# Performance work log

Hardware: AMD Instinct MI355X
Metric: run time of the kernel (lower is better)

Reference implementation:

```python
import jax, jax.numpy as jnp
import numpy as np


def setup_inputs() -> dict:
    key = jax.random.key(0)
    B, L, H, D = 4, 4096, 8, 64
    sample_k = int(np.ceil(np.log(L)))  # factor=1 -> U_part = ceil(ln L_K) = 9
    k1, k2, k3, k4 = jax.random.split(key, 4)
    return {
        "queries": jax.random.normal(k1, (B, L, H, D), jnp.float32),
        "keys": jax.random.normal(k2, (B, L, H, D), jnp.float32),
        "values": jax.random.normal(k3, (B, L, H, D), jnp.float32),
        "index_sample": jax.random.randint(k4, (L, sample_k), 0, L),
    }


def _prob_attention(Q, K, V, index_sample):
    # Q, K, V: [B, H, L, D]
    B, H, L_K, D = K.shape
    L_Q = Q.shape[2]
    u = min(int(np.ceil(np.log(L_Q))), L_Q)  # n_top (static)

    # --- _prob_QK: sampled scores, sparsity measure M, top-u queries ---
    # gather sampled keys per query position: [B, H, L_Q, sample_k, D]
    K_sample = K[:, :, index_sample, :]
    QK_sample = jnp.einsum('bhld,bhlsd->bhls', Q, K_sample)  # [B,H,L_Q,S]
    M = QK_sample.max(axis=-1) - QK_sample.sum(axis=-1) / L_K  # [B,H,L_Q]
    _, M_top = jax.lax.top_k(M, u)  # [B,H,u] indices of top queries

    Q_reduce = jnp.take_along_axis(Q, M_top[..., None], axis=2)  # [B,H,u,D]
    scale = 1.0 / jnp.sqrt(jnp.asarray(D, Q.dtype))
    scores = jnp.einsum('bhud,bhkd->bhuk', Q_reduce, K) * scale  # [B,H,u,L_K]

    # --- initial context (mask_flag=False): mean of V over keys ---
    context = jnp.broadcast_to(V.mean(axis=2, keepdims=True), (B, H, L_Q, D))

    # --- update context at the top-u query positions ---
    attn = jax.nn.softmax(scores, axis=-1)  # [B,H,u,L_K]
    ctx_top = jnp.einsum('bhuk,bhkd->bhud', attn, V)  # [B,H,u,D]
    b_idx = jnp.arange(B)[:, None, None]
    h_idx = jnp.arange(H)[None, :, None]
    context = context.at[b_idx, h_idx, M_top].set(ctx_top)
    return context, attn


def reference(queries, keys, values, index_sample):
    # inputs: [B, L, H, D] -> internal [B, H, L, D]
    Q = queries.transpose(0, 2, 1, 3)
    K = keys.transpose(0, 2, 1, 3)
    V = values.transpose(0, 2, 1, 3)
    context, attn = _prob_attention(Q, K, V, index_sample)
    return context.transpose(0, 2, 1, 3), attn
```

## Files before the change

kernel.cpp:

```cpp
#include <hip/hip_runtime.h>
#include <math.h>

#define B_ 4
#define L_ 4096
#define H_ 8
#define D_ 64
#define S_ 9
#define U_ 9
#define VC_ 64
#define NC_ 32
#define CC_ 16
#define TKC_ 8

#define MB2_ 8192
#define FILLBLK_ 8192

__device__ __forceinline__ float dot4(const float4& a, const float4& b) {
    return a.x * b.x + a.y * b.y + a.z * b.z + a.w * b.w;
}

__global__ void kernel_Mv(const float* __restrict__ Q, const float* __restrict__ K,
                          const int* __restrict__ idx, float* __restrict__ M,
                          const float* __restrict__ V, float* __restrict__ vpart) {
    __shared__ __align__(16) char smem[8192];
    int t = threadIdx.x;

    if (blockIdx.x >= MB2_) {
        int blk = blockIdx.x - MB2_;
        int c = blk & (VC_ - 1), b = blk >> 6;
        float4* red = (float4*)smem;
        float4 acc = make_float4(0.f, 0.f, 0.f, 0.f);
        int col = t & 127, lp = t >> 7;
        if (t < 512) {
            const float4* base = (const float4*)(V + (size_t)b * L_ * H_ * D_);
            for (int l = c * 64 + lp; l < (c + 1) * 64; l += 4) {
                float4 v = base[(size_t)l * 128 + col];
                acc.x += v.x; acc.y += v.y; acc.z += v.z; acc.w += v.w;
            }
            red[t] = acc;
        }
        __syncthreads();
        if (t < 128) {
            float4 r0 = red[t], r1 = red[t + 128], r2 = red[t + 256], r3 = red[t + 384];
            float4 o = make_float4(r0.x + r1.x + r2.x + r3.x, r0.y + r1.y + r2.y + r3.y,
                                   r0.z + r1.z + r2.z + r3.z, r0.w + r1.w + r2.w + r3.w);
            ((float4*)vpart)[(size_t)blk * 128 + t] = o;
        }
        return;
    }
    int n = blockIdx.x;
    int x = n & 7, m = n >> 3;
    int chunk = m & 255;
    int bh = (m >> 8) * 8 + x;
    int h = bh & (H_ - 1), b = bh >> 3;
    int l0 = chunk * 16;

    int j  = t & 3;
    int g  = t >> 2;
    int s  = g >> 4;
    int ll = g & 15;
    int l  = l0 + ll;

    int ki = idx[l * S_ + s];
    const float4* qb = (const float4*)(Q + (size_t)((b * L_ + l) * H_ + h) * D_);
    const float4* kb = (const float4*)(K + (size_t)((b * L_ + ki) * H_ + h) * D_);

    float acc = 0.0f;
#pragma unroll
    for (int c = 0; c < 4; ++c) acc += dot4(qb[j + 4 * c], kb[j + 4 * c]);
    acc += __shfl_xor(acc, 1);
    acc += __shfl_xor(acc, 2);

    float (*sdot)[S_] = (float (*)[S_])smem;
    if (j == 0) sdot[ll][s] = acc;
    __syncthreads();

    if (t < 16) {
        float mx = -INFINITY, sm = 0.0f;
#pragma unroll
        for (int ss = 0; ss < S_; ++ss) {
            float v = sdot[t][ss];
            mx = fmaxf(mx, v);
            sm += v;
        }
        M[((size_t)bh << 12) + l0 + t] = mx - sm * (1.0f / (float)L_);
    }
}

#define CSWAP(a, b)                                                          \
    if (v[b] > v[a] || (v[b] == v[a] && id[b] < id[a])) {                    \
        float tv = v[a]; v[a] = v[b]; v[b] = tv;                             \
        int ti = id[a]; id[a] = id[b]; id[b] = ti;                           \
    }

__global__ void kernel_topk(const float* __restrict__ M, int* __restrict__ Mtop,
                            const float* __restrict__ vpart, float* __restrict__ vmean) {
    int t = threadIdx.x;
    if (blockIdx.x >= 32) {
        int bh = blockIdx.x - 32;
        if (t < 64) {
            int h = bh & (H_ - 1), b = bh >> 3;
            float s = 0.0f;
            for (int c = 0; c < VC_; ++c)
                s += vpart[(size_t)(b * VC_ + c) * (H_ * D_) + h * D_ + t];
            vmean[bh * D_ + t] = s * (1.0f / (float)L_);
        }
        return;
    }
    int bh = blockIdx.x;
    int w = t >> 6, lane = t & 63;
    __shared__ float cvs[TKC_ * U_];
    __shared__ int   cis[TKC_ * U_];
    const float* Ms = M + ((size_t)bh << 12);

    {
        float v[8]; int id[8];
#pragma unroll
        for (int c = 0; c < 8; ++c) {
            int gi = w * 512 + lane + 64 * c;
            v[c] = Ms[gi]; id[c] = gi;
        }
        CSWAP(0,1) CSWAP(2,3) CSWAP(4,5) CSWAP(6,7)
        CSWAP(0,2) CSWAP(1,3) CSWAP(4,6) CSWAP(5,7)
        CSWAP(1,2) CSWAP(5,6)
        CSWAP(0,4) CSWAP(1,5) CSWAP(2,6) CSWAP(3,7)
        CSWAP(2,4) CSWAP(3,5)
        CSWAP(1,2) CSWAP(3,4) CSWAP(5,6)
#pragma unroll
        for (int r = 0; r < U_; ++r) {
            float bv = v[0]; int bi = id[0];
#pragma unroll
            for (int off = 1; off < 64; off <<= 1) {
                float ov = __shfl_xor(bv, off);
                int   oi = __shfl_xor(bi, off);
                if (ov > bv || (ov == bv && oi < bi)) { bv = ov; bi = oi; }
            }
            if (lane == 0) { cvs[w * U_ + r] = bv; cis[w * U_ + r] = bi; }
            if (id[0] == bi) {
#pragma unroll
                for (int c = 0; c < 7; ++c) { v[c] = v[c+1]; id[c] = id[c+1]; }
                v[7] = -INFINITY; id[7] = 0x7fffffff;
            }
        }
    }
    __syncthreads();
    if (w == 0) {
        float v[2]; int id[2];
        v[0] = cvs[lane]; id[0] = cis[lane];
        if (lane < TKC_ * U_ - 64) { v[1] = cvs[64 + lane]; id[1] = cis[64 + lane]; }
        else { v[1] = -INFINITY; id[1] = 0x7fffffff; }
        CSWAP(0,1)
#pragma unroll
        for (int r = 0; r < U_; ++r) {
            float bv = v[0]; int bi = id[0];
#pragma unroll
            for (int off = 1; off < 64; off <<= 1) {
                float ov = __shfl_xor(bv, off);
                int   oi = __shfl_xor(bi, off);
                if (ov > bv || (ov == bv && oi < bi)) { bv = ov; bi = oi; }
            }
            if (lane == 0) Mtop[bh * U_ + r] = bi;
            if (id[0] == bi) { v[0] = v[1]; id[0] = id[1]; v[1] = -INFINITY; id[1] = 0x7fffffff; }
        }
    }
}

__global__ void kernel_fill_scores(float* __restrict__ out, const float* __restrict__ vmean,
                                   const float* __restrict__ Q, const float* __restrict__ K,
                                   const int* __restrict__ Mtop, float* __restrict__ raw,
                                   float* __restrict__ spart) {
    int t = threadIdx.x;
    if (blockIdx.x < FILLBLK_) {
        int i = blockIdx.x * 256 + t;
        int d4 = i & 15;
        int h  = (i >> 4) & (H_ - 1);
        int l  = (i >> 7) & (L_ - 1);
        int b  = i >> 19;
        int bh = b * H_ + h;
        bool top = false;
#pragma unroll
        for (int u = 0; u < U_; ++u) top |= (Mtop[bh * U_ + u] == l);
        float4 w = top ? make_float4(0.f, 0.f, 0.f, 0.f)
                       : ((const float4*)vmean)[bh * 16 + d4];
        ((float4*)out)[i] = w;
        return;
    }
    int n = blockIdx.x - FILLBLK_;
    int x = n & 7, m = n >> 3;
    int chunk = m & (NC_ - 1);
    int bh = (m >> 5) * 8 + x;
    int h = bh & (H_ - 1), b = bh >> 3;
    int k0 = chunk * (L_ / NC_);

    __shared__ float qs[U_][D_];
    __shared__ float wsum[4][U_];
    if (t < 144) {
        int u = t / 16, c = t & 15;
        int l = Mtop[bh * U_ + u];
        ((float4*)qs[u])[c] =
            ((const float4*)(Q + (size_t)((b * L_ + l) * H_ + h) * D_))[c];
    }
    __syncthreads();

    int j = t & 3, g = t >> 2;
    float el[U_];
#pragma unroll
    for (int u = 0; u < U_; ++u) el[u] = 0.0f;

#pragma unroll
    for (int kk = 0; kk < 2; ++kk) {
        int k = k0 + g + 64 * kk;
        const float4* kb = (const float4*)(K + (size_t)((b * L_ + k) * H_ + h) * D_);
        float4 kv[4];
#pragma unroll
        for (int c = 0; c < 4; ++c) kv[c] = kb[j + 4 * c];
#pragma unroll
        for (int u = 0; u < U_; ++u) {
            float acc = 0.0f;
#pragma unroll
            for (int c = 0; c < 4; ++c)
                acc += dot4(((const float4*)qs[u])[j + 4 * c], kv[c]);
            acc += __shfl_xor(acc, 1);
            acc += __shfl_xor(acc, 2);
            float e = expf(acc * 0.125f);
            el[u] += e;
            if (j == 0) raw[((size_t)bh * U_ + u) * L_ + k] = e;
        }
    }
    int wv = t >> 6, lane = t & 63;
#pragma unroll
    for (int u = 0; u < U_; ++u) {
        float e = el[u];
#pragma unroll
        for (int off = 1; off < 64; off <<= 1)
            e += __shfl_xor(e, off);
        if (lane == 0) wsum[wv][u] = e * 0.25f;
    }
    __syncthreads();
    if (t < U_) {
        float s = wsum[0][t] + wsum[1][t] + wsum[2][t] + wsum[3][t];
        spart[(size_t)(bh * U_ + t) * NC_ + chunk] = s;
    }
}

__global__ void kernel_ctxf(float* __restrict__ attn, const float* __restrict__ V,
                            const int* __restrict__ Mtop, const float* __restrict__ spart,
                            float* __restrict__ out) {
    int n = blockIdx.x;
    int x = n & 7, m = n >> 3;
    int chunk = m & (CC_ - 1);
    int bh = (m >> 4) * 8 + x;
    int h = bh & (H_ - 1), b = bh >> 3;
    int k0 = chunk * (L_ / CC_);
    int t = threadIdx.x;

    __shared__ float sA[U_][256];
    __shared__ float4 red4[U_][4][16];
    __shared__ float sinvL[U_];

    if (t < U_) {
        const float* sp = spart + (size_t)(bh * U_ + t) * NC_;
        float s = 0.0f;
#pragma unroll
        for (int c = 0; c < NC_; ++c) s += sp[c];
        sinvL[t] = 1.0f / s;
    }
    __syncthreads();

    float* abase = attn + (size_t)bh * U_ * L_;
#pragma unroll
    for (int u = 0; u < U_; ++u) {
        float e = abase[(size_t)u * L_ + k0 + t] * sinvL[u];
        abase[(size_t)u * L_ + k0 + t] = e;
        sA[u][t] = e;
    }
    __syncthreads();

    int g = t >> 6, lane = t & 63;
    int kl = lane >> 4, d4 = lane & 15;

    float4 acc[U_];
#pragma unroll
    for (int u = 0; u < U_; ++u) acc[u] = make_float4(0.f, 0.f, 0.f, 0.f);

    for (int i = 0; i < 16; ++i) {
        int kloc = (g * 4 + kl) + 16 * i;
        float4 vv = *(const float4*)(V + (size_t)((b * L_ + k0 + kloc) * H_ + h) * D_ + 4 * d4);
#pragma unroll
        for (int u = 0; u < U_; ++u) {
            float av = sA[u][kloc];
            acc[u].x += av * vv.x; acc[u].y += av * vv.y;
            acc[u].z += av * vv.z; acc[u].w += av * vv.w;
        }
    }
#pragma unroll
    for (int u = 0; u < U_; ++u) {
        acc[u].x += __shfl_xor(acc[u].x, 16); acc[u].y += __shfl_xor(acc[u].y, 16);
        acc[u].z += __shfl_xor(acc[u].z, 16); acc[u].w += __shfl_xor(acc[u].w, 16);
        acc[u].x += __shfl_xor(acc[u].x, 32); acc[u].y += __shfl_xor(acc[u].y, 32);
        acc[u].z += __shfl_xor(acc[u].z, 32); acc[u].w += __shfl_xor(acc[u].w, 32);
    }
    if (kl == 0) {
#pragma unroll
        for (int u = 0; u < U_; ++u) red4[u][g][d4] = acc[u];
    }
    __syncthreads();
    if (t < U_ * 16) {
        int u = t >> 4, dd = t & 15;
        float4 s0 = red4[u][0][dd], s1 = red4[u][1][dd];
        float4 s2 = red4[u][2][dd], s3 = red4[u][3][dd];
        int lq = Mtop[bh * U_ + u];
        float* o = out + (size_t)((b * L_ + lq) * H_ + h) * D_ + 4 * dd;
        atomicAdd(o + 0, s0.x + s1.x + s2.x + s3.x);
        atomicAdd(o + 1, s0.y + s1.y + s2.y + s3.y);
        atomicAdd(o + 2, s0.z + s1.z + s2.z + s3.z);
        atomicAdd(o + 3, s0.w + s1.w + s2.w + s3.w);
    }
}

extern "C" void kernel_launch(void* const* d_in, const int* in_sizes, int n_in,
                              void* d_out, int out_size, void* d_ws, size_t ws_size,
                              hipStream_t stream) {
    const float* Q   = (const float*)d_in[0];
    const float* K   = (const float*)d_in[1];
    const float* V   = (const float*)d_in[2];
    const int*   idx = (const int*)d_in[3];

    float* ctx_out  = (float*)d_out;
    float* attn_out = (float*)d_out + (size_t)B_ * L_ * H_ * D_;

    float* M      = (float*)d_ws;
    float* vpart  = M + (size_t)B_ * H_ * L_;
    float* vmean  = vpart + (size_t)B_ * VC_ * H_ * D_;
    int*   Mtop   = (int*)(vmean + B_ * H_ * D_);
    float* spart  = (float*)(Mtop + 32 * U_);

    kernel_Mv<<<MB2_ + B_ * VC_, 576, 0, stream>>>(Q, K, idx, M, V, vpart);
    kernel_topk<<<64, 512, 0, stream>>>(M, Mtop, vpart, vmean);
    kernel_fill_scores<<<FILLBLK_ + 32 * NC_, 256, 0, stream>>>(
        ctx_out, vmean, Q, K, Mtop, attn_out, spart);
    kernel_ctxf<<<32 * CC_, 256, 0, stream>>>(attn_out, V, Mtop, spart, ctx_out);
}
```

Baseline: 233.9 us.

## Fuse score and context kernels using last-block-done normalization

Merges the score/exp kernel with the attention-times-V context kernel. Each score block now computes the unnormalized exp weights times V for its key chunk and atomically accumulates the result into a workspace buffer. An atomic counter lets the last block per (b,h) normalize the attention rows and write the final context rows. This removes one kernel launch and the separate re-read of attention scores, but the last block now rescales all 9x4096 attention values for its head on its own, which serializes that tail work. The fill path also skips the store for top query rows, and the zeroing of the accumulators and counters is folded into the topk kernel.

Result: slower. 270.1 us (+15.5%).

```diff
diff --git a/kernel.cpp b/kernel.cpp
--- a/kernel.cpp
+++ b/kernel.cpp
@@ -9,10 +9,10 @@
 #define U_ 9
 #define VC_ 64
 #define NC_ 32
-#define CC_ 16
 #define TKC_ 8
 
 #define MB2_ 8192
+#define SCBLK_ 1024
 #define FILLBLK_ 8192
 
 __device__ __forceinline__ float dot4(const float4& a, const float4& b) {
@@ -94,8 +94,14 @@
     }
 
 __global__ void kernel_topk(const float* __restrict__ M, int* __restrict__ Mtop,
-                            const float* __restrict__ vpart, float* __restrict__ vmean) {
+                            const float* __restrict__ vpart, float* __restrict__ vmean,
+                            float* __restrict__ ctxacc, int* __restrict__ counters) {
     int t = threadIdx.x;
+    {
+        int zi = blockIdx.x * 288 + t;
+        if (t < 288) ctxacc[zi] = 0.0f;
+        if (blockIdx.x == 0 && t < 32) counters[t] = 0;
+    }
     if (blockIdx.x >= 32) {
         int bh = blockIdx.x - 32;
         if (t < 64) {
@@ -165,13 +171,14 @@
     }
 }
 
-__global__ void kernel_fill_scores(float* __restrict__ out, const float* __restrict__ vmean,
-                                   const float* __restrict__ Q, const float* __restrict__ K,
-                                   const int* __restrict__ Mtop, float* __restrict__ raw,
-                                   float* __restrict__ spart) {
+__global__ void kernel_fsc(float* __restrict__ out, const float* __restrict__ vmean,
+                           const float* __restrict__ Q, const float* __restrict__ K,
+                           const float* __restrict__ V, const int* __restrict__ Mtop,
+                           float* __restrict__ attn, float* __restrict__ spart,
+                           float* __restrict__ ctxacc, int* __restrict__ counters) {
     int t = threadIdx.x;
-    if (blockIdx.x < FILLBLK_) {
-        int i = blockIdx.x * 256 + t;
+    if (blockIdx.x >= SCBLK_) {
+        int i = (blockIdx.x - SCBLK_) * 256 + t;
         int d4 = i & 15;
         int h  = (i >> 4) & (H_ - 1);
         int l  = (i >> 7) & (L_ - 1);
@@ -180,12 +187,11 @@
         bool top = false;
 #pragma unroll
         for (int u = 0; u < U_; ++u) top |= (Mtop[bh * U_ + u] == l);
-        float4 w = top ? make_float4(0.f, 0.f, 0.f, 0.f)
-                       : ((const float4*)vmean)[bh * 16 + d4];
-        ((float4*)out)[i] = w;
+        if (!top)
+            ((float4*)out)[i] = ((const float4*)vmean)[bh * 16 + d4];
         return;
     }
-    int n = blockIdx.x - FILLBLK_;
+    int n = blockIdx.x;
     int x = n & 7, m = n >> 3;
     int chunk = m & (NC_ - 1);
     int bh = (m >> 5) * 8 + x;
@@ -193,7 +199,12 @@
     int k0 = chunk * (L_ / NC_);
 
     __shared__ float qs[U_][D_];
+    __shared__ float sA[U_][128];
     __shared__ float wsum[4][U_];
+    __shared__ float4 red4[U_][4][16];
+    __shared__ float sinvL[U_];
+    __shared__ int isLast;
+
     if (t < 144) {
         int u = t / 16, c = t & 15;
         int l = Mtop[bh * U_ + u];
@@ -206,7 +217,6 @@
     float el[U_];
 #pragma unroll
     for (int u = 0; u < U_; ++u) el[u] = 0.0f;
-
 #pragma unroll
     for (int kk = 0; kk < 2; ++kk) {
         int k = k0 + g + 64 * kk;
@@ -224,67 +234,35 @@
             acc += __shfl_xor(acc, 2);
             float e = expf(acc * 0.125f);
             el[u] += e;
-            if (j == 0) raw[((size_t)bh * U_ + u) * L_ + k] = e;
-        }
-    }
-    int wv = t >> 6, lane = t & 63;
-#pragma unroll
-    for (int u = 0; u < U_; ++u) {
-        float e = el[u];
-#pragma unroll
-        for (int off = 1; off < 64; off <<= 1)
-            e += __shfl_xor(e, off);
-        if (lane == 0) wsum[wv][u] = e * 0.25f;
-    }
-    __syncthreads();
-    if (t < U_) {
-        float s = wsum[0][t] + wsum[1][t] + wsum[2][t] + wsum[3][t];
-        spart[(size_t)(bh * U_ + t) * NC_ + chunk] = s;
-    }
-}
-
-__global__ void kernel_ctxf(float* __restrict__ attn, const float* __restrict__ V,
-                            const int* __restrict__ Mtop, const float* __restrict__ spart,
-                            float* __restrict__ out) {
-    int n = blockIdx.x;
-    int x = n & 7, m = n >> 3;
-    int chunk = m & (CC_ - 1);
-    int bh = (m >> 4) * 8 + x;
-    int h = bh & (H_ - 1), b = bh >> 3;
-    int k0 = chunk * (L_ / CC_);
-    int t = threadIdx.x;
-
-    __shared__ float sA[U_][256];
-    __shared__ float4 red4[U_][4][16];
-    __shared__ float sinvL[U_];
-
-    if (t < U_) {
-        const float* sp = spart + (size_t)(bh * U_ + t) * NC_;
-        float s = 0.0f;
-#pragma unroll
-        for (int c = 0; c < NC_; ++c) s += sp[c];
-        sinvL[t] = 1.0f / s;
-    }
-    __syncthreads();
-
-    float* abase = attn + (size_t)bh * U_ * L_;
-#pragma unroll
-    for (int u = 0; u < U_; ++u) {
-        float e = abase[(size_t)u * L_ + k0 + t] * sinvL[u];
-        abase[(size_t)u * L_ + k0 + t] = e;
-        sA[u][t] = e;
-    }
-    __syncthreads();
-
-    int g = t >> 6, lane = t & 63;
+            if (j == 0) {
+                attn[((size_t)bh * U_ + u) * L_ + k] = e;
+                sA[u][g + 64 * kk] = e;
+            }
+        }
+    }
+    {
+        int wv = t >> 6, lane = t & 63;
+#pragma unroll
+        for (int u = 0; u < U_; ++u) {
+            float e = el[u];
+#pragma unroll
+            for (int off = 1; off < 64; off <<= 1)
+                e += __shfl_xor(e, off);
+            if (lane == 0) wsum[wv][u] = e * 0.25f;
+        }
+    }
+    __syncthreads();
+    if (t < U_)
+        spart[(size_t)(bh * U_ + t) * NC_ + chunk] =
+            wsum[0][t] + wsum[1][t] + wsum[2][t] + wsum[3][t];
+
+    int g2 = t >> 6, lane = t & 63;
     int kl = lane >> 4, d4 = lane & 15;
-
     float4 acc[U_];
 #pragma unroll
     for (int u = 0; u < U_; ++u) acc[u] = make_float4(0.f, 0.f, 0.f, 0.f);
-
-    for (int i = 0; i < 16; ++i) {
-        int kloc = (g * 4 + kl) + 16 * i;
+    for (int i = 0; i < 8; ++i) {
+        int kloc = (g2 * 4 + kl) + 16 * i;
         float4 vv = *(const float4*)(V + (size_t)((b * L_ + k0 + kloc) * H_ + h) * D_ + 4 * d4);
 #pragma unroll
         for (int u = 0; u < U_; ++u) {
@@ -302,19 +280,55 @@
     }
     if (kl == 0) {
 #pragma unroll
-        for (int u = 0; u < U_; ++u) red4[u][g][d4] = acc[u];
+        for (int u = 0; u < U_; ++u) red4[u][g2][d4] = acc[u];
     }
     __syncthreads();
     if (t < U_ * 16) {
         int u = t >> 4, dd = t & 15;
         float4 s0 = red4[u][0][dd], s1 = red4[u][1][dd];
         float4 s2 = red4[u][2][dd], s3 = red4[u][3][dd];
+        float* ca = ctxacc + ((size_t)bh * U_ + u) * 64 + 4 * dd;
+        atomicAdd(ca + 0, s0.x + s1.x + s2.x + s3.x);
+        atomicAdd(ca + 1, s0.y + s1.y + s2.y + s3.y);
+        atomicAdd(ca + 2, s0.z + s1.z + s2.z + s3.z);
+        atomicAdd(ca + 3, s0.w + s1.w + s2.w + s3.w);
+    }
+    __syncthreads();
+    if (t == 0) {
+        __threadfence();
+        int old = atomicAdd(&counters[bh], 1);
+        isLast = (old == NC_ - 1);
+    }
+    __syncthreads();
+    if (!isLast) return;
+
+    __threadfence();
+    if (t < U_) {
+        const float* sp = spart + (size_t)(bh * U_ + t) * NC_;
+        float s = 0.0f;
+#pragma unroll
+        for (int c = 0; c < NC_; ++c) s += sp[c];
+        sinvL[t] = 1.0f / s;
+    }
+    __syncthreads();
+    float* ab = attn + (size_t)bh * U_ * L_;
+#pragma unroll
+    for (int r = 0; r < U_; ++r) {
+        float sv = sinvL[r];
+        float4* row = (float4*)(ab + (size_t)r * L_);
+        for (int i = t; i < L_ / 4; i += 256) {
+            float4 v = row[i];
+            v.x *= sv; v.y *= sv; v.z *= sv; v.w *= sv;
+            row[i] = v;
+        }
+    }
+    if (t < U_ * 16) {
+        int u = t >> 4, dd = t & 15;
+        float sv = sinvL[u];
+        const float* ca = ctxacc + ((size_t)bh * U_ + u) * 64 + 4 * dd;
+        float4 c = make_float4(ca[0] * sv, ca[1] * sv, ca[2] * sv, ca[3] * sv);
         int lq = Mtop[bh * U_ + u];
-        float* o = out + (size_t)((b * L_ + lq) * H_ + h) * D_ + 4 * dd;
-        atomicAdd(o + 0, s0.x + s1.x + s2.x + s3.x);
-        atomicAdd(o + 1, s0.y + s1.y + s2.y + s3.y);
-        atomicAdd(o + 2, s0.z + s1.z + s2.z + s3.z);
-        atomicAdd(o + 3, s0.w + s1.w + s2.w + s3.w);
+        *(float4*)(out + (size_t)((b * L_ + lq) * H_ + h) * D_ + 4 * dd) = c;
     }
 }
 
@@ -329,15 +343,16 @@
     float* ctx_out  = (float*)d_out;
     float* attn_out = (float*)d_out + (size_t)B_ * L_ * H_ * D_;
 
-    float* M      = (float*)d_ws;
-    float* vpart  = M + (size_t)B_ * H_ * L_;
-    float* vmean  = vpart + (size_t)B_ * VC_ * H_ * D_;
-    int*   Mtop   = (int*)(vmean + B_ * H_ * D_);
-    float* spart  = (float*)(Mtop + 32 * U_);
+    float* M       = (float*)d_ws;
+    float* vpart   = M + (size_t)B_ * H_ * L_;
+    float* vmean   = vpart + (size_t)B_ * VC_ * H_ * D_;
+    int*   Mtop    = (int*)(vmean + B_ * H_ * D_);
+    float* spart   = (float*)(Mtop + 32 * U_);
+    float* ctxacc  = spart + (size_t)32 * U_ * NC_;
+    int*   counters= (int*)(ctxacc + 32 * U_ * 64);
 
     kernel_Mv<<<MB2_ + B_ * VC_, 576, 0, stream>>>(Q, K, idx, M, V, vpart);
-    kernel_topk<<<64, 512, 0, stream>>>(M, Mtop, vpart, vmean);
-    kernel_fill_scores<<<FILLBLK_ + 32 * NC_, 256, 0, stream>>>(
-        ctx_out, vmean, Q, K, Mtop, attn_out, spart);
-    kernel_ctxf<<<32 * CC_, 256, 0, stream>>>(attn_out, V, Mtop, spart, ctx_out);
-}
+    kernel_topk<<<64, 512, 0, stream>>>(M, Mtop, vpart, vmean, ctxacc, counters);
+    kernel_fsc<<<SCBLK_ + FILLBLK_, 256, 0, stream>>>(
+        ctx_out, vmean, Q, K, V, Mtop, attn_out, spart, ctxacc, counters);
+}
```
